# Optimization experiments

Measured on AMD Instinct MI355X. Metric: run time of the kernel, lower is better.

Reference implementation:

```python
import jax, jax.numpy as jnp
import numpy as np


def setup_inputs() -> dict:
    key = jax.random.key(0)
    embeddings = jax.random.normal(key, (4, 2048, 128), dtype=jnp.float32)
    return {"embeddings": embeddings}


def _pairwise_dist(x):
    # x: [N, D] -> Euclidean distance matrix [N, N] (matches torch.cdist, p=2)
    sq = jnp.sum(x * x, axis=-1)  # [N]
    d2 = sq[:, None] + sq[None, :] - 2.0 * (x @ x.T)
    d2 = jnp.maximum(d2, 0.0)
    # safe sqrt: exact 0 on the diagonal / coincident points, no NaN grads
    safe = jnp.where(d2 > 0.0, d2, 1.0)
    return jnp.where(d2 > 0.0, jnp.sqrt(safe), 0.0)


def reference(embeddings) -> jnp.ndarray:
    b, s, d = embeddings.shape
    x = embeddings.reshape(b * s, d)
    dist = _pairwise_dist(x)                 # [N, N]
    mean_dist = jnp.mean(dist)
    # torch.std default: unbiased (ddof=1) over all elements
    std_dist = jnp.std(dist, ddof=1)
    return std_dist / (mean_dist + 1e-08)
```

## Files before the change

kernel.cpp:

```cpp
#include <hip/hip_runtime.h>
#include <hip/hip_bf16.h>
#include <math.h>


#define NPTS   8192
#define DIM    128
#define TIL    128
#define NGRID  (NPTS / TIL)
#define NTOT   (NGRID * (NGRID + 1) / 2)
#define NPREP  (NPTS / 32)
#define NTILES (NPTS / 128)
#define NTOTSQ (NTILES * NTILES)

typedef __attribute__((ext_vector_type(8))) short short8;
typedef __attribute__((ext_vector_type(4))) float f32x4;

typedef const __attribute__((address_space(1))) void* gas_ptr;
typedef __attribute__((address_space(3))) void* las_ptr;

__device__ __forceinline__ void gload16(const void* g, void* l) {
    __builtin_amdgcn_global_load_lds((gas_ptr)g, (las_ptr)l, 16, 0, 0);
}
__device__ __forceinline__ float fsqrt(float x) {
    return __builtin_amdgcn_sqrtf(x);
}

__global__ __launch_bounds__(256)
void ph_prep(const float* __restrict__ x, ushort* __restrict__ xb,
             float* __restrict__ sq, float* __restrict__ cs_part)
{
    __shared__ float xs[32][129];
    const int tid = threadIdx.x;
    const int rw  = tid >> 3;
    const int row = blockIdx.x * 32 + rw;
    const int seg = tid & 7;
    const float4* p = reinterpret_cast<const float4*>(x + (size_t)row * DIM + seg * 16);
    float v[16];
    {
        float4 a = p[0], b = p[1], c = p[2], d = p[3];
        v[0]=a.x; v[1]=a.y; v[2]=a.z; v[3]=a.w;  v[4]=b.x; v[5]=b.y; v[6]=b.z; v[7]=b.w;
        v[8]=c.x; v[9]=c.y; v[10]=c.z; v[11]=c.w; v[12]=d.x; v[13]=d.y; v[14]=d.z; v[15]=d.w;
    }
    float s = 0.f;
    ushort h[16];
#pragma unroll
    for (int j = 0; j < 16; ++j) {
        __hip_bfloat16 hb = __float2bfloat16(v[j]);
        h[j] = *reinterpret_cast<ushort*>(&hb);
        s = fmaf(v[j], v[j], s);
        xs[rw][seg * 16 + j] = v[j];
    }
    short8 o0, o1;
#pragma unroll
    for (int j = 0; j < 8; ++j) { o0[j] = (short)h[j]; o1[j] = (short)h[j+8]; }
    short8* dst = reinterpret_cast<short8*>(xb + (size_t)row * DIM + seg * 16);
    dst[0] = o0; dst[1] = o1;
    s += __shfl_xor(s, 1); s += __shfl_xor(s, 2); s += __shfl_xor(s, 4);
    if (seg == 0) sq[row] = s;
    __syncthreads();
    if (tid < DIM) {
        float c = 0.f;
#pragma unroll 8
        for (int r = 0; r < 32; ++r) c += xs[r][tid];
        cs_part[blockIdx.x * DIM + tid] = c;
    }
}

__global__ __launch_bounds__(256, 4)
void ph_gram(const ushort* __restrict__ xb, const float* __restrict__ sq,
             double* __restrict__ partials)
{
    const int f   = blockIdx.x;
    const int tid = threadIdx.x;

    int bi = (int)((129.0f - fsqrt((float)(16641 - 8 * f))) * 0.5f);
    while ((bi + 1) * 64 - ((bi + 1) * bi) / 2 <= f) ++bi;
    while (bi * 64 - (bi * (bi - 1)) / 2 > f) --bi;
    const int bj = bi + (f - (bi * 64 - (bi * (bi - 1)) / 2));

    __shared__ ushort Ah[TIL * 64];
    __shared__ ushort Bh[TIL * 64];
    __shared__ double rr[4];

    const int lane = tid & 63;
    const int wv   = tid >> 6;
    const int wr   = wv >> 1;
    const int wc   = wv & 1;

    const char* gA = (const char*)(xb + (size_t)bi * TIL * DIM);
    const char* gB = (const char*)(xb + (size_t)bj * TIL * DIM);

    const int srow = lane >> 3;
    const int skb  = (lane & 7) * 16;

#define STAGE(h)                                                              \
    {                                                                         \
        _Pragma("unroll")                                                     \
        for (int c = 0; c < 4; ++c) {                                         \
            const int chunk = wv * 4 + c;                                     \
            const int row   = chunk * 8 + srow;                               \
            const size_t go = (size_t)row * 256 + (h) * 128                   \
                              + (skb ^ ((row & 7) << 4));                     \
            gload16(gA + go, (char*)Ah + chunk * 1024);                       \
            gload16(gB + go, (char*)Bh + chunk * 1024);                       \
        }                                                                     \
    }

    f32x4 acc[4][4];
#pragma unroll
    for (int m = 0; m < 4; ++m)
#pragma unroll
        for (int n = 0; n < 4; ++n) acc[m][n] = (f32x4){0.f, 0.f, 0.f, 0.f};

#define COMPUTE()                                                             \
    {                                                                         \
        _Pragma("unroll")                                                     \
        for (int ks = 0; ks < 2; ++ks) {                                      \
            const int kb = ks * 64 + (lane >> 4) * 16;                        \
            short8 af[4], bfr[4];                                             \
            _Pragma("unroll")                                                 \
            for (int m = 0; m < 4; ++m) {                                     \
                const int row = wr * 64 + m * 16 + (lane & 15);               \
                af[m] = *reinterpret_cast<const short8*>(                     \
                    (const char*)Ah + row * 128 + (kb ^ ((row & 7) << 4)));   \
            }                                                                 \
            _Pragma("unroll")                                                 \
            for (int n = 0; n < 4; ++n) {                                     \
                const int col = wc * 64 + n * 16 + (lane & 15);               \
                bfr[n] = *reinterpret_cast<const short8*>(                    \
                    (const char*)Bh + col * 128 + (kb ^ ((col & 7) << 4)));   \
            }                                                                 \
            __builtin_amdgcn_s_setprio(1);                                    \
            _Pragma("unroll")                                                 \
            for (int m = 0; m < 4; ++m)                                       \
                _Pragma("unroll")                                             \
                for (int n = 0; n < 4; ++n)                                   \
                    acc[m][n] = __builtin_amdgcn_mfma_f32_16x16x32_bf16(      \
                        af[m], bfr[n], acc[m][n], 0, 0, 0);                   \
            __builtin_amdgcn_s_setprio(0);                                    \
        }                                                                     \
    }

    STAGE(0);
    __syncthreads();
    COMPUTE();
    __syncthreads();
    STAGE(1);
    __syncthreads();
    COMPUTE();

    const float* sqA = sq + bi * TIL + wr * 64 + (lane >> 4) * 4;
    const float* sqB = sq + bj * TIL + wc * 64 + (lane & 15);
    float nb[4];
#pragma unroll
    for (int n = 0; n < 4; ++n) nb[n] = sqB[n * 16];

    float s1a = 0.f, s1b = 0.f, s1c = 0.f, s1d = 0.f;
    const bool diag = (bi == bj);
    if (!diag) {
#pragma unroll
        for (int m = 0; m < 4; ++m) {
            const float4 v = *reinterpret_cast<const float4*>(sqA + m * 16);
#pragma unroll
            for (int n = 0; n < 4; ++n) {
                s1a += fsqrt(fmaxf(fmaf(-2.f, acc[m][n][0], v.x + nb[n]), 0.f));
                s1b += fsqrt(fmaxf(fmaf(-2.f, acc[m][n][1], v.y + nb[n]), 0.f));
                s1c += fsqrt(fmaxf(fmaf(-2.f, acc[m][n][2], v.z + nb[n]), 0.f));
                s1d += fsqrt(fmaxf(fmaf(-2.f, acc[m][n][3], v.w + nb[n]), 0.f));
            }
        }
    } else {
#pragma unroll
        for (int m = 0; m < 4; ++m) {
            const float4 v = *reinterpret_cast<const float4*>(sqA + m * 16);
            const float nav[4] = {v.x, v.y, v.z, v.w};
#pragma unroll
            for (int n = 0; n < 4; ++n) {
                const int col = wc * 64 + n * 16 + (lane & 15);
#pragma unroll
                for (int r = 0; r < 4; ++r) {
                    const int row = wr * 64 + m * 16 + (lane >> 4) * 4 + r;
                    float d = fmaxf(fmaf(-2.f, acc[m][n][r], nav[r] + nb[n]), 0.f);
                    if (row == col) d = 0.f;
                    s1a += fsqrt(d);
                }
            }
        }
    }
    float s1 = (s1a + s1b) + (s1c + s1d);
#pragma unroll
    for (int off = 1; off < 64; off <<= 1) s1 += __shfl_xor(s1, off);
    const double w = diag ? 1.0 : 2.0;
    if (lane == 0) rr[wv] = (double)s1 * w;
    __syncthreads();
    if (tid == 0) partials[f] = (rr[0] + rr[1]) + (rr[2] + rr[3]);
#undef STAGE
#undef COMPUTE
}

__global__ __launch_bounds__(256)
void ph_finalize(const double* __restrict__ partials, const float* __restrict__ sq,
                 const float* __restrict__ cs_part, float* __restrict__ out)
{
    __shared__ double r1[256], r2[256], r3[128];
    const int tid = threadIdx.x;
    double s1 = 0.0;
    for (int i = tid; i < NTOT; i += 256) s1 += partials[i];
    double sn = 0.0;
    for (int k = 0; k < NPTS / 256; ++k) sn += (double)sq[tid + k * 256];
    r1[tid] = s1; r2[tid] = sn;
    if (tid < DIM) {
        double c = 0.0;
        for (int b = 0; b < NPREP; ++b) c += (double)cs_part[b * DIM + tid];
        r3[tid] = c * c;
    }
    __syncthreads();
    for (int off = 128; off > 0; off >>= 1) {
        if (tid < off) { r1[tid] += r1[tid + off]; r2[tid] += r2[tid + off]; }
        __syncthreads();
    }
    for (int off = 64; off > 0; off >>= 1) {
        if (tid < off) r3[tid] += r3[tid + off];
        __syncthreads();
    }
    if (tid == 0) {
        const double M    = (double)NPTS * (double)NPTS;
        const double S1   = r1[0];
        const double S2   = 2.0 * (double)NPTS * r2[0] - 2.0 * r3[0];
        const double mean = S1 / M;
        double var = (S2 - S1 * S1 / M) / (M - 1.0);
        if (var < 0.0) var = 0.0;
        out[0] = (float)(sqrt(var) / (mean + 1e-8));
    }
}

#define LSTR 132
__global__ __launch_bounds__(256)
void ph_pair_kernel(const float* __restrict__ x, double* __restrict__ partials)
{
    const int bi  = blockIdx.y;
    const int bj  = blockIdx.x;
    const int tid = threadIdx.x;
    const int flat = bi * NTILES + bj;
    if (bj < bi) {
        if (tid == 0) { partials[2*flat] = 0.0; partials[2*flat+1] = 0.0; }
        return;
    }
    __shared__ __align__(16) float As[128 * LSTR];
    __shared__ __align__(16) float Bs[128 * LSTR];
    __shared__ float  nA[128];
    __shared__ float  nB[128];
    __shared__ double red1[256];
    __shared__ double red2[256];
    const float* Ab = x + (size_t)bi * 128 * DIM;
    const float* Bb = x + (size_t)bj * 128 * DIM;
#pragma unroll
    for (int it = 0; it < 16; ++it) {
        const int e   = (tid + it * 256) * 4;
        const int row = e >> 7;
        const int k   = e & 127;
        float4 va = *reinterpret_cast<const float4*>(Ab + e);
        As[(k+0)*LSTR + row] = va.x; As[(k+1)*LSTR + row] = va.y;
        As[(k+2)*LSTR + row] = va.z; As[(k+3)*LSTR + row] = va.w;
        float4 vb = *reinterpret_cast<const float4*>(Bb + e);
        Bs[(k+0)*LSTR + row] = vb.x; Bs[(k+1)*LSTR + row] = vb.y;
        Bs[(k+2)*LSTR + row] = vb.z; Bs[(k+3)*LSTR + row] = vb.w;
    }
    __syncthreads();
    if (tid < 128) {
        float s = 0.f;
#pragma unroll 8
        for (int k = 0; k < DIM; ++k) { float v = As[k*LSTR + tid]; s = fmaf(v, v, s); }
        nA[tid] = s;
    } else {
        const int r = tid - 128;
        float s = 0.f;
#pragma unroll 8
        for (int k = 0; k < DIM; ++k) { float v = Bs[k*LSTR + r]; s = fmaf(v, v, s); }
        nB[r] = s;
    }
    __syncthreads();
    const int tx = tid & 15, ty = tid >> 4;
    const int ra = ty * 8, cb = tx * 8;
    float acc[8][8];
#pragma unroll
    for (int r = 0; r < 8; ++r)
#pragma unroll
        for (int c = 0; c < 8; ++c) acc[r][c] = 0.f;
#pragma unroll 4
    for (int k = 0; k < DIM; ++k) {
        const float4 a0 = *reinterpret_cast<const float4*>(&As[k*LSTR + ra]);
        const float4 a1 = *reinterpret_cast<const float4*>(&As[k*LSTR + ra + 4]);
        const float4 b0 = *reinterpret_cast<const float4*>(&Bs[k*LSTR + cb]);
        const float4 b1 = *reinterpret_cast<const float4*>(&Bs[k*LSTR + cb + 4]);
        const float a[8] = {a0.x,a0.y,a0.z,a0.w,a1.x,a1.y,a1.z,a1.w};
        const float b[8] = {b0.x,b0.y,b0.z,b0.w,b1.x,b1.y,b1.z,b1.w};
#pragma unroll
        for (int r = 0; r < 8; ++r)
#pragma unroll
            for (int c = 0; c < 8; ++c)
                acc[r][c] = fmaf(a[r], b[c], acc[r][c]);
    }
    double s1 = 0.0, s2 = 0.0;
    const int gi0 = bi*128 + ra, gj0 = bj*128 + cb;
#pragma unroll
    for (int r = 0; r < 8; ++r) {
#pragma unroll
        for (int c = 0; c < 8; ++c) {
            float d2 = nA[ra+r] + nB[cb+c] - 2.0f * acc[r][c];
            d2 = fmaxf(d2, 0.0f);
            if (gi0 + r == gj0 + c) d2 = 0.0f;
            s1 += (double)sqrtf(d2);
            s2 += (double)d2;
        }
    }
    const double w = (bi == bj) ? 1.0 : 2.0;
    s1 *= w; s2 *= w;
    red1[tid] = s1; red2[tid] = s2;
    __syncthreads();
    for (int off = 128; off > 0; off >>= 1) {
        if (tid < off) { red1[tid] += red1[tid+off]; red2[tid] += red2[tid+off]; }
        __syncthreads();
    }
    if (tid == 0) { partials[2*flat] = red1[0]; partials[2*flat+1] = red2[0]; }
}

__global__ __launch_bounds__(256)
void ph_finalize_sq(const double* __restrict__ partials, float* __restrict__ out)
{
    __shared__ double r1[256], r2[256];
    const int tid = threadIdx.x;
    double s1 = 0.0, s2 = 0.0;
    for (int i = tid; i < NTOTSQ; i += 256) { s1 += partials[2*i]; s2 += partials[2*i+1]; }
    r1[tid] = s1; r2[tid] = s2;
    __syncthreads();
    for (int off = 128; off > 0; off >>= 1) {
        if (tid < off) { r1[tid] += r1[tid+off]; r2[tid] += r2[tid+off]; }
        __syncthreads();
    }
    if (tid == 0) {
        const double M    = (double)NPTS * (double)NPTS;
        const double mean = r1[0] / M;
        double var = (r2[0] - r1[0]*r1[0]/M) / (M - 1.0);
        if (var < 0.0) var = 0.0;
        out[0] = (float)(sqrt(var) / (mean + 1e-8));
    }
}

extern "C" void kernel_launch(void* const* d_in, const int* in_sizes, int n_in,
                              void* d_out, int out_size, void* d_ws, size_t ws_size,
                              hipStream_t stream)
{
    const float* x = (const float*)d_in[0];
    float* out     = (float*)d_out;

    const size_t XB_OFF = 0;
    const size_t SQ_OFF = (size_t)NPTS * DIM * sizeof(ushort);
    const size_t CS_OFF = SQ_OFF + NPTS * sizeof(float);
    const size_t PT_OFF = CS_OFF + (size_t)NPREP * DIM * sizeof(float);
    const size_t NEEDED = PT_OFF + (size_t)NTOT * sizeof(double);

    if (ws_size >= NEEDED) {
        ushort* xb       = (ushort*)((char*)d_ws + XB_OFF);
        float*  sq       = (float*) ((char*)d_ws + SQ_OFF);
        float*  cs_part  = (float*) ((char*)d_ws + CS_OFF);
        double* partials = (double*)((char*)d_ws + PT_OFF);

        ph_prep<<<NPREP, 256, 0, stream>>>(x, xb, sq, cs_part);
        ph_gram<<<NTOT, 256, 0, stream>>>(xb, sq, partials);
        ph_finalize<<<1, 256, 0, stream>>>(partials, sq, cs_part, out);
    } else {
        double* partials = (double*)d_ws;
        ph_pair_kernel<<<dim3(NTILES, NTILES), 256, 0, stream>>>(x, partials);
        ph_finalize_sq<<<1, 256, 0, stream>>>(partials, out);
    }
}
```

Baseline: 35.47 us.

## Make gram kernel persistent over 4-5 tile pairs with double-buffered B and register-resident A

Changes ph_gram from one block per upper-triangular tile pair (2080 blocks) to 512 blocks. Each block walks 4-5 consecutive pairs. The A slab's fragments are held in registers and reloaded only when the row slab changes. The B tile is double-buffered in LDS so the next pair's load overlaps the current MFMA and sqrt epilogue. This aims to cut launch and block-start overhead, redundant A loads and non-overlapped load latency, at the cost of more registers, 64KB LDS per block and lower occupancy (launch bounds 2).

Result: slower. 38.58 us (+8.8%).

```diff
diff --git a/kernel.cpp b/kernel.cpp
--- a/kernel.cpp
+++ b/kernel.cpp
@@ -6,8 +6,9 @@
 #define NPTS   8192
 #define DIM    128
 #define TIL    128
-#define NGRID  (NPTS / TIL)
-#define NTOT   (NGRID * (NGRID + 1) / 2)
+#define NSLAB  (NPTS / TIL)
+#define NPAIR  (NSLAB * (NSLAB + 1) / 2)
+#define NBLKS  512
 #define NPREP  (NPTS / 32)
 #define NTILES (NPTS / 128)
 #define NTOTSQ (NTILES * NTILES)
@@ -66,69 +67,72 @@
     }
 }
 
-__global__ __launch_bounds__(256, 4)
+__global__ __launch_bounds__(256, 2)
 void ph_gram(const ushort* __restrict__ xb, const float* __restrict__ sq,
              double* __restrict__ partials)
 {
-    const int f   = blockIdx.x;
-    const int tid = threadIdx.x;
-
-    int bi = (int)((129.0f - fsqrt((float)(16641 - 8 * f))) * 0.5f);
-    while ((bi + 1) * 64 - ((bi + 1) * bi) / 2 <= f) ++bi;
-    while (bi * 64 - (bi * (bi - 1)) / 2 > f) --bi;
-    const int bj = bi + (f - (bi * 64 - (bi * (bi - 1)) / 2));
-
-    __shared__ ushort Ah[TIL * 64];
-    __shared__ ushort Bh[TIL * 64];
-    __shared__ double rr[4];
-
+    const int b    = blockIdx.x;
+    const int tid  = threadIdx.x;
     const int lane = tid & 63;
     const int wv   = tid >> 6;
     const int wr   = wv >> 1;
     const int wc   = wv & 1;
 
-    const char* gA = (const char*)(xb + (size_t)bi * TIL * DIM);
-    const char* gB = (const char*)(xb + (size_t)bj * TIL * DIM);
-
-    const int srow = lane >> 3;
-    const int skb  = (lane & 7) * 16;
-
-#define STAGE(h)                                                              \
+    __shared__ ushort Bbuf[2][TIL * DIM];
+    __shared__ double rr[4];
+
+    const int pstart = 4 * b + (b < 32 ? b : 32);
+    const int pcnt   = 4 + (b < 32 ? 1 : 0);
+
+    int p  = pstart;
+    int si = (int)((129.0f - fsqrt((float)(16641 - 8 * p))) * 0.5f);
+    while ((si + 1) * 64 - ((si + 1) * si) / 2 <= p) ++si;
+    while (si * 64 - (si * (si - 1)) / 2 > p) --si;
+    int tj = si + (p - (si * 64 - (si * (si - 1)) / 2));
+
+    short8 af[4][4];
+    float4 na4[4];
+
+#define LOADA(s_)                                                             \
+    {                                                                         \
+        const char* ga = (const char*)xb +                                    \
+            ((size_t)(s_) * TIL + wr * 64 + (lane & 15)) * 256;               \
+        _Pragma("unroll")                                                     \
+        for (int m = 0; m < 4; ++m)                                           \
+            _Pragma("unroll")                                                 \
+            for (int ks = 0; ks < 4; ++ks)                                    \
+                af[m][ks] = *reinterpret_cast<const short8*>(                 \
+                    ga + m * 16 * 256 + ks * 64 + (lane >> 4) * 16);          \
+        const float* sa = sq + (s_) * TIL + wr * 64 + (lane >> 4) * 4;        \
+        _Pragma("unroll")                                                     \
+        for (int m = 0; m < 4; ++m)                                           \
+            na4[m] = *reinterpret_cast<const float4*>(sa + m * 16);           \
+    }
+
+#define STAGEB(t_, buf_)                                                      \
+    {                                                                         \
+        const char* gb = (const char*)xb + (size_t)(t_) * TIL * 256;          \
+        char* dst_ = (char*)(buf_);                                           \
+        _Pragma("unroll")                                                     \
+        for (int i = 0; i < 8; ++i) {                                         \
+            const int row = i * 16 + (tid >> 4);                              \
+            const int kbl = ((tid & 15) * 16) ^ ((row & 7) << 4);             \
+            gload16(gb + (size_t)row * 256 + kbl, dst_ + i * 4096 + tid * 16);\
+        }                                                                     \
+    }
+
+    f32x4 acc[4][4];
+#define COMPUTEP(buf_)                                                        \
     {                                                                         \
         _Pragma("unroll")                                                     \
-        for (int c = 0; c < 4; ++c) {                                         \
-            const int chunk = wv * 4 + c;                                     \
-            const int row   = chunk * 8 + srow;                               \
-            const size_t go = (size_t)row * 256 + (h) * 128                   \
-                              + (skb ^ ((row & 7) << 4));                     \
-            gload16(gA + go, (char*)Ah + chunk * 1024);                       \
-            gload16(gB + go, (char*)Bh + chunk * 1024);                       \
-        }                                                                     \
-    }
-
-    f32x4 acc[4][4];
-#pragma unroll
-    for (int m = 0; m < 4; ++m)
-#pragma unroll
-        for (int n = 0; n < 4; ++n) acc[m][n] = (f32x4){0.f, 0.f, 0.f, 0.f};
-
-#define COMPUTE()                                                             \
-    {                                                                         \
-        _Pragma("unroll")                                                     \
-        for (int ks = 0; ks < 2; ++ks) {                                      \
+        for (int ks = 0; ks < 4; ++ks) {                                      \
             const int kb = ks * 64 + (lane >> 4) * 16;                        \
-            short8 af[4], bfr[4];                                             \
-            _Pragma("unroll")                                                 \
-            for (int m = 0; m < 4; ++m) {                                     \
-                const int row = wr * 64 + m * 16 + (lane & 15);               \
-                af[m] = *reinterpret_cast<const short8*>(                     \
-                    (const char*)Ah + row * 128 + (kb ^ ((row & 7) << 4)));   \
-            }                                                                 \
+            short8 bfr[4];                                                    \
             _Pragma("unroll")                                                 \
             for (int n = 0; n < 4; ++n) {                                     \
                 const int col = wc * 64 + n * 16 + (lane & 15);               \
                 bfr[n] = *reinterpret_cast<const short8*>(                    \
-                    (const char*)Bh + col * 128 + (kb ^ ((col & 7) << 4)));   \
+                    (const char*)(buf_) + col * 256 + (kb ^ ((col & 7) << 4)));\
             }                                                                 \
             __builtin_amdgcn_s_setprio(1);                                    \
             _Pragma("unroll")                                                 \
@@ -136,66 +140,82 @@
                 _Pragma("unroll")                                             \
                 for (int n = 0; n < 4; ++n)                                   \
                     acc[m][n] = __builtin_amdgcn_mfma_f32_16x16x32_bf16(      \
-                        af[m], bfr[n], acc[m][n], 0, 0, 0);                   \
+                        af[m][ks], bfr[n], acc[m][n], 0, 0, 0);               \
             __builtin_amdgcn_s_setprio(0);                                    \
         }                                                                     \
     }
 
-    STAGE(0);
-    __syncthreads();
-    COMPUTE();
-    __syncthreads();
-    STAGE(1);
-    __syncthreads();
-    COMPUTE();
-
-    const float* sqA = sq + bi * TIL + wr * 64 + (lane >> 4) * 4;
-    const float* sqB = sq + bj * TIL + wc * 64 + (lane & 15);
-    float nb[4];
-#pragma unroll
-    for (int n = 0; n < 4; ++n) nb[n] = sqB[n * 16];
-
-    float s1a = 0.f, s1b = 0.f, s1c = 0.f, s1d = 0.f;
-    const bool diag = (bi == bj);
-    if (!diag) {
-#pragma unroll
-        for (int m = 0; m < 4; ++m) {
-            const float4 v = *reinterpret_cast<const float4*>(sqA + m * 16);
-#pragma unroll
-            for (int n = 0; n < 4; ++n) {
-                s1a += fsqrt(fmaxf(fmaf(-2.f, acc[m][n][0], v.x + nb[n]), 0.f));
-                s1b += fsqrt(fmaxf(fmaf(-2.f, acc[m][n][1], v.y + nb[n]), 0.f));
-                s1c += fsqrt(fmaxf(fmaf(-2.f, acc[m][n][2], v.z + nb[n]), 0.f));
-                s1d += fsqrt(fmaxf(fmaf(-2.f, acc[m][n][3], v.w + nb[n]), 0.f));
+    LOADA(si);
+    STAGEB(tj, Bbuf[0]);
+    __syncthreads();
+
+    int   asi = si, csi = si, ctj = tj, cur = 0;
+    float sOa = 0.f, sOb = 0.f, sOc = 0.f, sOd = 0.f;
+    float sD  = 0.f;
+
+    for (int it = 0; it < pcnt; ++it) {
+        int nsi = csi, ntj = ctj + 1;
+        if (ntj == NSLAB) { ++nsi; ntj = nsi; }
+        if (it + 1 < pcnt) STAGEB(ntj, Bbuf[cur ^ 1]);
+        if (csi != asi) { LOADA(csi); asi = csi; }
+
+#pragma unroll
+        for (int m = 0; m < 4; ++m)
+#pragma unroll
+            for (int n = 0; n < 4; ++n) acc[m][n] = (f32x4){0.f, 0.f, 0.f, 0.f};
+
+        COMPUTEP(Bbuf[cur]);
+
+        const float* sqB = sq + ctj * TIL + wc * 64 + (lane & 15);
+        float nb[4];
+#pragma unroll
+        for (int n = 0; n < 4; ++n) nb[n] = sqB[n * 16];
+
+        if (csi != ctj) {
+#pragma unroll
+            for (int m = 0; m < 4; ++m) {
+                const float4 v = na4[m];
+#pragma unroll
+                for (int n = 0; n < 4; ++n) {
+                    sOa += fsqrt(fmaxf(fmaf(-2.f, acc[m][n][0], v.x + nb[n]), 0.f));
+                    sOb += fsqrt(fmaxf(fmaf(-2.f, acc[m][n][1], v.y + nb[n]), 0.f));
+                    sOc += fsqrt(fmaxf(fmaf(-2.f, acc[m][n][2], v.z + nb[n]), 0.f));
+                    sOd += fsqrt(fmaxf(fmaf(-2.f, acc[m][n][3], v.w + nb[n]), 0.f));
+                }
             }
-        }
-    } else {
-#pragma unroll
-        for (int m = 0; m < 4; ++m) {
-            const float4 v = *reinterpret_cast<const float4*>(sqA + m * 16);
-            const float nav[4] = {v.x, v.y, v.z, v.w};
-#pragma unroll
-            for (int n = 0; n < 4; ++n) {
-                const int col = wc * 64 + n * 16 + (lane & 15);
-#pragma unroll
-                for (int r = 0; r < 4; ++r) {
-                    const int row = wr * 64 + m * 16 + (lane >> 4) * 4 + r;
-                    float d = fmaxf(fmaf(-2.f, acc[m][n][r], nav[r] + nb[n]), 0.f);
-                    if (row == col) d = 0.f;
-                    s1a += fsqrt(d);
+        } else {
+#pragma unroll
+            for (int m = 0; m < 4; ++m) {
+                const float4 v = na4[m];
+                const float nav[4] = {v.x, v.y, v.z, v.w};
+#pragma unroll
+                for (int n = 0; n < 4; ++n) {
+                    const int col = wc * 64 + n * 16 + (lane & 15);
+#pragma unroll
+                    for (int r = 0; r < 4; ++r) {
+                        const int row = wr * 64 + m * 16 + (lane >> 4) * 4 + r;
+                        float d = fmaxf(fmaf(-2.f, acc[m][n][r], nav[r] + nb[n]), 0.f);
+                        if (row == col) d = 0.f;
+                        sD += fsqrt(d);
+                    }
                 }
             }
         }
-    }
-    float s1 = (s1a + s1b) + (s1c + s1d);
+
+        __syncthreads();
+        cur ^= 1;
+        csi = nsi; ctj = ntj;
+    }
+
+    float s1 = sD + 2.f * ((sOa + sOb) + (sOc + sOd));
 #pragma unroll
     for (int off = 1; off < 64; off <<= 1) s1 += __shfl_xor(s1, off);
-    const double w = diag ? 1.0 : 2.0;
-    if (lane == 0) rr[wv] = (double)s1 * w;
-    __syncthreads();
-    if (tid == 0) partials[f] = (rr[0] + rr[1]) + (rr[2] + rr[3]);
-#undef STAGE
-#undef COMPUTE
+    if (lane == 0) rr[wv] = (double)s1;
+    __syncthreads();
+    if (tid == 0) partials[b] = (rr[0] + rr[1]) + (rr[2] + rr[3]);
+#undef LOADA
+#undef STAGEB
+#undef COMPUTEP
 }
 
 __global__ __launch_bounds__(256)
@@ -205,7 +225,7 @@
     __shared__ double r1[256], r2[256], r3[128];
     const int tid = threadIdx.x;
     double s1 = 0.0;
-    for (int i = tid; i < NTOT; i += 256) s1 += partials[i];
+    for (int i = tid; i < NBLKS; i += 256) s1 += partials[i];
     double sn = 0.0;
     for (int k = 0; k < NPTS / 256; ++k) sn += (double)sq[tid + k * 256];
     r1[tid] = s1; r2[tid] = sn;
@@ -358,7 +378,7 @@
     const size_t SQ_OFF = (size_t)NPTS * DIM * sizeof(ushort);
     const size_t CS_OFF = SQ_OFF + NPTS * sizeof(float);
     const size_t PT_OFF = CS_OFF + (size_t)NPREP * DIM * sizeof(float);
-    const size_t NEEDED = PT_OFF + (size_t)NTOT * sizeof(double);
+    const size_t NEEDED = PT_OFF + (size_t)NBLKS * sizeof(double);
 
     if (ws_size >= NEEDED) {
         ushort* xb       = (ushort*)((char*)d_ws + XB_OFF);
@@ -367,7 +387,7 @@
         double* partials = (double*)((char*)d_ws + PT_OFF);
 
         ph_prep<<<NPREP, 256, 0, stream>>>(x, xb, sq, cs_part);
-        ph_gram<<<NTOT, 256, 0, stream>>>(xb, sq, partials);
+        ph_gram<<<NBLKS, 256, 0, stream>>>(xb, sq, partials);
         ph_finalize<<<1, 256, 0, stream>>>(partials, sq, cs_part, out);
     } else {
         double* partials = (double*)d_ws;
```
